# Kernel tuning notes

Hardware: AMD Instinct MI355X
Metric: run time of the kernel (lower is better)

## Reference

```python
import jax, jax.numpy as jnp
import numpy as np

N_NODES = 100000
D_IN = 128
H_DIM = 128
N_EDGES = 1600000


def _gcn_conv(x, src, dst, dinv, W, b):
    # PyG GCNConv(improved=True): h = x @ W; out = A_hat h + b,
    # A_hat = D^{-1/2} (A + 2I) D^{-1/2}
    h = x @ W                                   # [N, H]
    norm = dinv[src] * dinv[dst]                # [E]
    agg = jnp.zeros_like(h).at[dst].add(h[src] * norm[:, None])
    agg = agg + h * (2.0 * dinv * dinv)[:, None]  # self-loop, weight 2.0
    return agg + b


def setup_inputs() -> dict:
    key = jax.random.key(0)
    ks = jax.random.split(key, 12)
    s = 1.0 / np.sqrt(D_IN)
    sh = 1.0 / np.sqrt(2 * H_DIM)
    inp = {
        "x": jax.random.normal(ks[0], (N_NODES, D_IN), jnp.float32),
        "edge_index": jax.random.randint(ks[1], (2, N_EDGES), 0, N_NODES, jnp.int64),
        # GCNConv weights (in -> hidden), bias
        "Wz": jax.random.uniform(ks[2], (D_IN, H_DIM), jnp.float32, -s, s),
        "bz": jnp.zeros((H_DIM,), jnp.float32),
        "Wr": jax.random.uniform(ks[3], (D_IN, H_DIM), jnp.float32, -s, s),
        "br": jnp.zeros((H_DIM,), jnp.float32),
        "Wh": jax.random.uniform(ks[4], (D_IN, H_DIM), jnp.float32, -s, s),
        "bh": jnp.zeros((H_DIM,), jnp.float32),
        # TGCN gate linears: Linear(2h, h)
        "lzW": jax.random.uniform(ks[5], (2 * H_DIM, H_DIM), jnp.float32, -sh, sh),
        "lzb": jax.random.uniform(ks[6], (H_DIM,), jnp.float32, -sh, sh),
        "lrW": jax.random.uniform(ks[7], (2 * H_DIM, H_DIM), jnp.float32, -sh, sh),
        "lrb": jax.random.uniform(ks[8], (H_DIM,), jnp.float32, -sh, sh),
        "lhW": jax.random.uniform(ks[9], (2 * H_DIM, H_DIM), jnp.float32, -sh, sh),
        "lhb": jax.random.uniform(ks[10], (H_DIM,), jnp.float32, -sh, sh),
        # final linear2: hidden -> 1
        "W2": jax.random.uniform(ks[11], (H_DIM, 1), jnp.float32, -1 / np.sqrt(H_DIM), 1 / np.sqrt(H_DIM)),
        "b2": jnp.zeros((1,), jnp.float32),
    }
    return inp


def reference(x, edge_index, Wz, bz, Wr, br, Wh, bh, lzW, lzb, lrW, lrb, lhW, lhb, W2, b2):
    src, dst = edge_index[0], edge_index[1]
    n = x.shape[0]
    # improved GCN norm: deg includes self-loop weight 2
    deg = jnp.zeros((n,), x.dtype).at[dst].add(jnp.ones_like(src, x.dtype)) + 2.0
    dinv = jnp.where(deg > 0, deg ** -0.5, 0.0)
    # TGCN cell with H0 = 0
    H0 = jnp.zeros((n, Wz.shape[1]), x.dtype)
    Z = jax.nn.sigmoid(jnp.concatenate([_gcn_conv(x, src, dst, dinv, Wz, bz), H0], axis=1) @ lzW + lzb)
    R = jax.nn.sigmoid(jnp.concatenate([_gcn_conv(x, src, dst, dinv, Wr, br), H0], axis=1) @ lrW + lrb)
    Ht = jnp.tanh(jnp.concatenate([_gcn_conv(x, src, dst, dinv, Wh, bh), H0 * R], axis=1) @ lhW + lhb)
    H = Z * H0 + (1.0 - Z) * Ht
    # forward: relu output is discarded (y = h overwrites), then linear2
    return H @ W2 + b2
```

## Files before the change

kernel.cpp:

```cpp
#include <hip/hip_runtime.h>
#include <math.h>

#define D 128
#define BSHIFT 9
#define CAP 12288
#define EPT 13
#define P1B 481
#define XCB 12500

typedef __attribute__((ext_vector_type(8))) short s8v;
typedef __attribute__((ext_vector_type(8))) unsigned short us8;
typedef __attribute__((ext_vector_type(4))) unsigned short us4;
typedef __attribute__((ext_vector_type(4))) float f4v;

__device__ __forceinline__ float bf2f(unsigned short u) {
    union { unsigned int i; float f; } v; v.i = ((unsigned int)u) << 16; return v.f;
}
__device__ __forceinline__ unsigned short f2bf(float f) {
    union { float f; unsigned int i; } v; v.f = f;
    unsigned int r = v.i + 0x7FFFu + ((v.i >> 16) & 1u);
    return (unsigned short)(r >> 16);
}

__global__ __launch_bounds__(256) void k_combo(
    const int* __restrict__ src, const int* __restrict__ dst, int E,
    int* __restrict__ bcur, unsigned long long* __restrict__ pairs,
    const float* __restrict__ x, unsigned short* __restrict__ xb, int n4,
    const float* __restrict__ Wz, const float* __restrict__ bz,
    const float* __restrict__ lzW, const float* __restrict__ lzb,
    const float* __restrict__ Wh, const float* __restrict__ bh,
    const float* __restrict__ lhW, const float* __restrict__ lhb,
    unsigned short* __restrict__ Mt, float* __restrict__ c) {
    __shared__ int cnt[256];
    __shared__ int base[256];
    int bx = blockIdx.x, tid = threadIdx.x;

    if (bx < P1B) {
        int ed[EPT], es[EPT], rk[EPT];
        int e0 = bx * (EPT * 256) + tid;
        cnt[tid] = 0;
        __syncthreads();
        #pragma unroll
        for (int i = 0; i < EPT; ++i) {
            int e = e0 + i * 256;
            bool ok = e < E;
            ed[i] = ok ? dst[e] : 0;
            es[i] = ok ? src[e] : 0;
            rk[i] = ok ? atomicAdd(&cnt[ed[i] >> BSHIFT], 1) : 0;
        }
        __syncthreads();
        if (cnt[tid] > 0) base[tid] = tid * CAP + atomicAdd(&bcur[tid], cnt[tid]);
        __syncthreads();
        #pragma unroll
        for (int i = 0; i < EPT; ++i) {
            int e = e0 + i * 256;
            if (e < E) {
                int bk = ed[i] >> BSHIFT;
                pairs[base[bk] + rk[i]] =
                    ((unsigned long long)(unsigned int)ed[i] << 32) | (unsigned int)es[i];
            }
        }
    } else if (bx < P1B + XCB) {
        int i = (bx - P1B) * 256 + tid;
        if (i < n4) {
            float4 v = ((const float4*)x)[i];
            us4 o;
            o[0] = f2bf(v.x); o[1] = f2bf(v.y); o[2] = f2bf(v.z); o[3] = f2bf(v.w);
            ((us4*)xb)[i] = o;
        }
    } else {
        int k = bx - (P1B + XCB);
        int j = tid;
        int jj = j & 127;
        const float* W = (j < 128) ? Wz : Wh;
        const float* L = (j < 128) ? lzW : lhW;
        float s = 0.f;
        for (int t = 0; t < 128; ++t) s += W[k * 128 + t] * L[t * 128 + jj];
        Mt[(size_t)j * 128 + k] = f2bf(s);
        if (k == 0) {
            const float* b  = (j < 128) ? bz  : bh;
            const float* lb = (j < 128) ? lzb : lhb;
            float cs = lb[jj];
            for (int t = 0; t < 128; ++t) cs += b[t] * L[t * 128 + jj];
            c[j] = cs;
        }
    }
}

__global__ __launch_bounds__(256) void k_part2(const unsigned long long* __restrict__ pairs,
                                               const int* __restrict__ bcur,
                                               int NB, int N, int E,
                                               int* __restrict__ rowptr,
                                               float* __restrict__ dinv,
                                               int* __restrict__ esrc) {
    __shared__ int cnt[512];
    __shared__ int lcur[512];
    __shared__ int ts[256];
    int b = blockIdx.x, tid = threadIdx.x;
    int n0 = b << BSHIFT;
    int nn = min(N - n0, 1 << BSHIFT);
    int tot = bcur[b];
    long pbase = (long)b * CAP;

    ts[tid] = (tid < b) ? bcur[tid] : 0;
    __syncthreads();
    for (int off = 128; off > 0; off >>= 1) {
        if (tid < off) ts[tid] += ts[tid + off];
        __syncthreads();
    }
    int obase = ts[0];
    __syncthreads();

    cnt[tid] = 0; cnt[tid + 256] = 0;
    __syncthreads();
    for (int i = tid; i < tot; i += 256)
        atomicAdd(&cnt[(int)(pairs[pbase + i] >> 32) - n0], 1);
    __syncthreads();

    int a0 = cnt[2 * tid], a1 = cnt[2 * tid + 1];
    int s = a0 + a1;
    ts[tid] = s; __syncthreads();
    for (int off = 1; off < 256; off <<= 1) {
        int add = (tid >= off) ? ts[tid - off] : 0;
        __syncthreads();
        ts[tid] += add;
        __syncthreads();
    }
    int excl = ts[tid] - s;
    lcur[2 * tid]     = obase + excl;
    lcur[2 * tid + 1] = obase + excl + a0;
    if (2 * tid < nn) {
        rowptr[n0 + 2 * tid] = obase + excl;
        dinv[n0 + 2 * tid]   = rsqrtf((float)a0 + 2.0f);
    }
    if (2 * tid + 1 < nn) {
        rowptr[n0 + 2 * tid + 1] = obase + excl + a0;
        dinv[n0 + 2 * tid + 1]   = rsqrtf((float)a1 + 2.0f);
    }
    if (b == 0 && tid == 0) rowptr[N] = E;
    __syncthreads();

    for (int i = tid; i < tot; i += 256) {
        unsigned long long p = pairs[pbase + i];
        int dl = (int)(p >> 32) - n0;
        int pos = atomicAdd(&lcur[dl], 1);
        esrc[pos] = (int)(p & 0xffffffffu);
    }
}

#define ASTRIDE 136
__global__ __launch_bounds__(256, 4) void k_gather_ep(
    const unsigned short* __restrict__ xb,
    const int* __restrict__ esrc,
    const int* __restrict__ rowptr,
    const float* __restrict__ dinv,
    const unsigned short* __restrict__ Mt,
    const float* __restrict__ c, const float* __restrict__ W2,
    const float* __restrict__ b2, float* __restrict__ out, int N) {
    __shared__ unsigned short Ast[64 * ASTRIDE];
    __shared__ float pbuf[4][64];

    int tid = threadIdx.x;
    int n0 = blockIdx.x * 64;
    int hw = tid >> 5;
    int sub = tid & 31;
    int eo = sub >> 4, cs = sub & 15;

    for (int rep = 0; rep < 8; ++rep) {
        int node = n0 + rep * 8 + hw;
        int row = rep * 8 + hw;
        if (node < N) {
            int start = rowptr[node], end = rowptr[node + 1];
            float dd = dinv[node];
            float acc[8];
            #pragma unroll
            for (int j = 0; j < 8; ++j) acc[j] = 0.f;
            for (int base = start; base < end; base += 32) {
                int cntv = min(32, end - base);
                int myedge = 0; float mynorm = 0.f;
                if (sub < cntv) { myedge = esrc[base + sub]; mynorm = dinv[myedge]; }
                int pr = (cntv + 1) >> 1;
                int i = 0;
                for (; i + 3 < pr; i += 4) {
                    int i0 = 2 * i + eo;
                    int   s0 = __shfl(myedge, i0,     32); float w0 = __shfl(mynorm, i0,     32);
                    int   s1 = __shfl(myedge, i0 + 2, 32); float w1 = __shfl(mynorm, i0 + 2, 32);
                    int   s2 = __shfl(myedge, i0 + 4, 32); float w2 = __shfl(mynorm, i0 + 4, 32);
                    int   s3 = __shfl(myedge, i0 + 6, 32); float w3 = __shfl(mynorm, i0 + 6, 32);
                    us8 v0 = *(const us8*)(xb + (size_t)s0 * D + cs * 8);
                    us8 v1 = *(const us8*)(xb + (size_t)s1 * D + cs * 8);
                    us8 v2 = *(const us8*)(xb + (size_t)s2 * D + cs * 8);
                    us8 v3 = *(const us8*)(xb + (size_t)s3 * D + cs * 8);
                    #pragma unroll
                    for (int j = 0; j < 8; ++j) acc[j] += bf2f(v0[j]) * w0;
                    #pragma unroll
                    for (int j = 0; j < 8; ++j) acc[j] += bf2f(v1[j]) * w1;
                    #pragma unroll
                    for (int j = 0; j < 8; ++j) acc[j] += bf2f(v2[j]) * w2;
                    #pragma unroll
                    for (int j = 0; j < 8; ++j) acc[j] += bf2f(v3[j]) * w3;
                }
                for (; i < pr; ++i) {
                    int i0 = 2 * i + eo;
                    int   s0 = __shfl(myedge, i0, 32); float w0 = __shfl(mynorm, i0, 32);
                    us8 v0 = *(const us8*)(xb + (size_t)s0 * D + cs * 8);
                    #pragma unroll
                    for (int j = 0; j < 8; ++j) acc[j] += bf2f(v0[j]) * w0;
                }
            }
            #pragma unroll
            for (int j = 0; j < 8; ++j) acc[j] += __shfl_xor(acc[j], 16);
            if (eo == 0) {
                us8 xs = *(const us8*)(xb + (size_t)node * D + cs * 8);
                float sfac = 2.f * dd * dd;
                us8 r;
                #pragma unroll
                for (int j = 0; j < 8; ++j) r[j] = f2bf(acc[j] * dd + bf2f(xs[j]) * sfac);
                *(us8*)&Ast[row * ASTRIDE + cs * 8] = r;
            }
        } else if (eo == 0) {
            us8 z = {0, 0, 0, 0, 0, 0, 0, 0};
            *(us8*)&Ast[row * ASTRIDE + cs * 8] = z;
        }
    }
    __syncthreads();

    int wv = tid >> 6;
    int lane = tid & 63;
    int l = lane & 15, q = lane >> 4;
    int tz0 = 2 * wv;
    f4v acc[4][4];
    #pragma unroll
    for (int i = 0; i < 4; ++i)
        #pragma unroll
        for (int nt = 0; nt < 4; ++nt) acc[i][nt] = (f4v){0.f, 0.f, 0.f, 0.f};

    const unsigned short* Bb = Mt + (size_t)l * 128 + q * 8;

    #pragma unroll
    for (int ks = 0; ks < 4; ++ks) {
        s8v b[4];
        #pragma unroll
        for (int i = 0; i < 2; ++i) {
            b[i]     = *(const s8v*)(Bb + (size_t)(tz0 + i) * 16 * 128 + ks * 32);
            b[2 + i] = *(const s8v*)(Bb + (size_t)(8 + tz0 + i) * 16 * 128 + ks * 32);
        }
        #pragma unroll
        for (int nt = 0; nt < 4; ++nt) {
            s8v a = *(const s8v*)&Ast[(nt * 16 + l) * ASTRIDE + ks * 32 + q * 8];
            #pragma unroll
            for (int i = 0; i < 4; ++i)
                acc[i][nt] = __builtin_amdgcn_mfma_f32_16x16x32_bf16(a, b[i], acc[i][nt], 0, 0, 0);
        }
    }

    float p[4][4];
    #pragma unroll
    for (int nt = 0; nt < 4; ++nt)
        #pragma unroll
        for (int r = 0; r < 4; ++r) p[nt][r] = 0.f;
    #pragma unroll
    for (int i = 0; i < 2; ++i) {
        int col = (tz0 + i) * 16 + l;
        float cz = c[col], ch = c[128 + col], w2 = W2[col];
        #pragma unroll
        for (int nt = 0; nt < 4; ++nt)
            #pragma unroll
            for (int r = 0; r < 4; ++r) {
                float gz = acc[i][nt][r] + cz;
                float gh = acc[2 + i][nt][r] + ch;
                float z  = 1.f / (1.f + __expf(-gz));
                float ht = 1.f - 2.f / (__expf(2.f * gh) + 1.f);
                p[nt][r] += (1.f - z) * ht * w2;
            }
    }
    #pragma unroll
    for (int nt = 0; nt < 4; ++nt)
        #pragma unroll
        for (int r = 0; r < 4; ++r) {
            p[nt][r] += __shfl_xor(p[nt][r], 1);
            p[nt][r] += __shfl_xor(p[nt][r], 2);
            p[nt][r] += __shfl_xor(p[nt][r], 4);
            p[nt][r] += __shfl_xor(p[nt][r], 8);
        }
    if (l == 0) {
        #pragma unroll
        for (int nt = 0; nt < 4; ++nt)
            #pragma unroll
            for (int r = 0; r < 4; ++r)
                pbuf[wv][nt * 16 + q * 4 + r] = p[nt][r];
    }
    __syncthreads();
    if (tid < 64) {
        int n = n0 + tid;
        if (n < N)
            out[n] = pbuf[0][tid] + pbuf[1][tid] + pbuf[2][tid] + pbuf[3][tid] + b2[0];
    }
}

extern "C" void kernel_launch(void* const* d_in, const int* in_sizes, int n_in,
                              void* d_out, int out_size, void* d_ws, size_t ws_size,
                              hipStream_t stream) {
    const float* x    = (const float*)d_in[0];
    const int*   eidx = (const int*)d_in[1];
    const float* Wz   = (const float*)d_in[2];
    const float* bz   = (const float*)d_in[3];
    const float* Wh   = (const float*)d_in[6];
    const float* bh   = (const float*)d_in[7];
    const float* lzW  = (const float*)d_in[8];
    const float* lzb  = (const float*)d_in[9];
    const float* lhW  = (const float*)d_in[12];
    const float* lhb  = (const float*)d_in[13];
    const float* W2   = (const float*)d_in[14];
    const float* b2   = (const float*)d_in[15];
    float* out = (float*)d_out;

    int N = in_sizes[0] / D;
    int E = in_sizes[1] / 2;
    const int* src = eidx;
    const int* dst = eidx + E;
    int NB = (N + (1 << BSHIFT) - 1) >> BSHIFT;

    char* ws = (char*)d_ws;
    size_t off = 0;
    auto alloc = [&](size_t bytes) { void* p = ws + off; off += (bytes + 511) & ~(size_t)511; return p; };
    unsigned short* xb = (unsigned short*)alloc((size_t)N * D * 2);
    unsigned long long* pairs = (unsigned long long*)alloc((size_t)NB * CAP * 8);
    int*   rowptr = (int*)  alloc((size_t)(N + 1) * 4);
    float* dinv   = (float*)alloc((size_t)N * 4);
    int*   esrc   = (int*)  alloc((size_t)E * 4);
    int*   bcur   = (int*)  alloc(256 * 4);
    unsigned short* Mt = (unsigned short*)alloc(256 * 128 * 2);
    float* c      = (float*)alloc(256 * 4);

    hipMemsetAsync(bcur, 0, 256 * sizeof(int), stream);

    int n4 = N * (D / 4);
    k_combo<<<P1B + XCB + 128, 256, 0, stream>>>(
        src, dst, E, bcur, pairs, x, xb, n4,
        Wz, bz, lzW, lzb, Wh, bh, lhW, lhb, Mt, c);
    k_part2<<<NB, 256, 0, stream>>>(pairs, bcur, NB, N, E, rowptr, dinv, esrc);
    k_gather_ep<<<(N + 63) / 64, 256, 0, stream>>>(
        xb, esrc, rowptr, dinv, Mt, c, W2, b2, out, N);
}
```

Before: 249.6 us.

## Pack edge pairs into 32 bits and split gather from MFMA epilogue

Edge (dst,src) pairs are packed into a single 32-bit word, holding the local dst offset and a 17-bit src, instead of 64 bits. This halves the traffic through the bucket scratch, which now reuses the xab buffer. The fused gather+MFMA kernel is split in two. A standalone gather kernel writes the aggregated bf16 rows to a global buffer, and a separate MFMA epilogue reads them back into shared memory. The split is meant to lift the occupancy limit the fused kernel placed on the gather, at the cost of an extra 25.6MB write and read and one more launch. The 17-bit src packing only holds for N below 131072.

```diff
diff --git a/kernel.cpp b/kernel.cpp
--- a/kernel.cpp
+++ b/kernel.cpp
@@ -24,7 +24,7 @@
 
 __global__ __launch_bounds__(256) void k_combo(
     const int* __restrict__ src, const int* __restrict__ dst, int E,
-    int* __restrict__ bcur, unsigned long long* __restrict__ pairs,
+    int* __restrict__ bcur, unsigned int* __restrict__ pairs,
     const float* __restrict__ x, unsigned short* __restrict__ xb, int n4,
     const float* __restrict__ Wz, const float* __restrict__ bz,
     const float* __restrict__ lzW, const float* __restrict__ lzb,
@@ -36,7 +36,7 @@
     int bx = blockIdx.x, tid = threadIdx.x;
 
     if (bx < P1B) {
-        int ed[EPT], es[EPT], rk[EPT];
+        unsigned int pk[EPT]; int rkbk[EPT];
         int e0 = bx * (EPT * 256) + tid;
         cnt[tid] = 0;
         __syncthreads();
@@ -44,9 +44,12 @@
         for (int i = 0; i < EPT; ++i) {
             int e = e0 + i * 256;
             bool ok = e < E;
-            ed[i] = ok ? dst[e] : 0;
-            es[i] = ok ? src[e] : 0;
-            rk[i] = ok ? atomicAdd(&cnt[ed[i] >> BSHIFT], 1) : 0;
+            int d = ok ? dst[e] : 0;
+            int s = ok ? src[e] : 0;
+            int bk = d >> BSHIFT;
+            pk[i] = ((unsigned int)(d & ((1 << BSHIFT) - 1)) << 17) | (unsigned int)s;
+            int r = ok ? atomicAdd(&cnt[bk], 1) : 0;
+            rkbk[i] = (bk << 16) | r;
         }
         __syncthreads();
         if (cnt[tid] > 0) base[tid] = tid * CAP + atomicAdd(&bcur[tid], cnt[tid]);
@@ -55,9 +58,8 @@
         for (int i = 0; i < EPT; ++i) {
             int e = e0 + i * 256;
             if (e < E) {
-                int bk = ed[i] >> BSHIFT;
-                pairs[base[bk] + rk[i]] =
-                    ((unsigned long long)(unsigned int)ed[i] << 32) | (unsigned int)es[i];
+                int bk = rkbk[i] >> 16;
+                pairs[base[bk] + (rkbk[i] & 0xffff)] = pk[i];
             }
         }
     } else if (bx < P1B + XCB) {
@@ -87,7 +89,7 @@
     }
 }
 
-__global__ __launch_bounds__(256) void k_part2(const unsigned long long* __restrict__ pairs,
+__global__ __launch_bounds__(256) void k_part2(const unsigned int* __restrict__ pairs,
                                                const int* __restrict__ bcur,
                                                int NB, int N, int E,
                                                int* __restrict__ rowptr,
@@ -114,7 +116,7 @@
     cnt[tid] = 0; cnt[tid + 256] = 0;
     __syncthreads();
     for (int i = tid; i < tot; i += 256)
-        atomicAdd(&cnt[(int)(pairs[pbase + i] >> 32) - n0], 1);
+        atomicAdd(&cnt[pairs[pbase + i] >> 17], 1);
     __syncthreads();
 
     int a0 = cnt[2 * tid], a1 = cnt[2 * tid + 1];
@@ -141,20 +143,76 @@
     __syncthreads();
 
     for (int i = tid; i < tot; i += 256) {
-        unsigned long long p = pairs[pbase + i];
-        int dl = (int)(p >> 32) - n0;
+        unsigned int p = pairs[pbase + i];
+        int dl = p >> 17;
         int pos = atomicAdd(&lcur[dl], 1);
-        esrc[pos] = (int)(p & 0xffffffffu);
+        esrc[pos] = (int)(p & 0x1FFFFu);
+    }
+}
+
+__global__ __launch_bounds__(256) void k_gather(const unsigned short* __restrict__ xb,
+                                                const int* __restrict__ esrc,
+                                                const int* __restrict__ rowptr,
+                                                const float* __restrict__ dinv,
+                                                unsigned short* __restrict__ xab, int N) {
+    int node = (blockIdx.x * blockDim.x + threadIdx.x) >> 5;
+    int sub  = threadIdx.x & 31;
+    if (node >= N) return;
+    int eo = sub >> 4, cs = sub & 15;
+    int start = rowptr[node], end = rowptr[node + 1];
+    float dd = dinv[node];
+    float acc[8];
+    #pragma unroll
+    for (int j = 0; j < 8; ++j) acc[j] = 0.f;
+
+    for (int base = start; base < end; base += 32) {
+        int cnt = min(32, end - base);
+        int myedge = 0; float mynorm = 0.f;
+        if (sub < cnt) { myedge = esrc[base + sub]; mynorm = dinv[myedge]; }
+        int pairs = (cnt + 1) >> 1;
+        int i = 0;
+        for (; i + 3 < pairs; i += 4) {
+            int i0 = 2 * i + eo;
+            int   s0 = __shfl(myedge, i0,     32); float w0 = __shfl(mynorm, i0,     32);
+            int   s1 = __shfl(myedge, i0 + 2, 32); float w1 = __shfl(mynorm, i0 + 2, 32);
+            int   s2 = __shfl(myedge, i0 + 4, 32); float w2 = __shfl(mynorm, i0 + 4, 32);
+            int   s3 = __shfl(myedge, i0 + 6, 32); float w3 = __shfl(mynorm, i0 + 6, 32);
+            us8 v0 = *(const us8*)(xb + (size_t)s0 * D + cs * 8);
+            us8 v1 = *(const us8*)(xb + (size_t)s1 * D + cs * 8);
+            us8 v2 = *(const us8*)(xb + (size_t)s2 * D + cs * 8);
+            us8 v3 = *(const us8*)(xb + (size_t)s3 * D + cs * 8);
+            #pragma unroll
+            for (int j = 0; j < 8; ++j) acc[j] += bf2f(v0[j]) * w0;
+            #pragma unroll
+            for (int j = 0; j < 8; ++j) acc[j] += bf2f(v1[j]) * w1;
+            #pragma unroll
+            for (int j = 0; j < 8; ++j) acc[j] += bf2f(v2[j]) * w2;
+            #pragma unroll
+            for (int j = 0; j < 8; ++j) acc[j] += bf2f(v3[j]) * w3;
+        }
+        for (; i < pairs; ++i) {
+            int i0 = 2 * i + eo;
+            int   s0 = __shfl(myedge, i0, 32); float w0 = __shfl(mynorm, i0, 32);
+            us8 v0 = *(const us8*)(xb + (size_t)s0 * D + cs * 8);
+            #pragma unroll
+            for (int j = 0; j < 8; ++j) acc[j] += bf2f(v0[j]) * w0;
+        }
+    }
+    #pragma unroll
+    for (int j = 0; j < 8; ++j) acc[j] += __shfl_xor(acc[j], 16);
+    if (eo == 0) {
+        us8 xs = *(const us8*)(xb + (size_t)node * D + cs * 8);
+        float sfac = 2.f * dd * dd;
+        us8 r;
+        #pragma unroll
+        for (int j = 0; j < 8; ++j) r[j] = f2bf(acc[j] * dd + bf2f(xs[j]) * sfac);
+        *(us8*)(xab + (size_t)node * D + cs * 8) = r;
     }
 }
 
 #define ASTRIDE 136
-__global__ __launch_bounds__(256, 4) void k_gather_ep(
-    const unsigned short* __restrict__ xb,
-    const int* __restrict__ esrc,
-    const int* __restrict__ rowptr,
-    const float* __restrict__ dinv,
-    const unsigned short* __restrict__ Mt,
+__global__ __launch_bounds__(256, 4) void k_ep_mfma(
+    const unsigned short* __restrict__ xab, const unsigned short* __restrict__ Mt,
     const float* __restrict__ c, const float* __restrict__ W2,
     const float* __restrict__ b2, float* __restrict__ out, int N) {
     __shared__ unsigned short Ast[64 * ASTRIDE];
@@ -162,72 +220,20 @@
 
     int tid = threadIdx.x;
     int n0 = blockIdx.x * 64;
-    int hw = tid >> 5;
-    int sub = tid & 31;
-    int eo = sub >> 4, cs = sub & 15;
-
-    for (int rep = 0; rep < 8; ++rep) {
-        int node = n0 + rep * 8 + hw;
-        int row = rep * 8 + hw;
-        if (node < N) {
-            int start = rowptr[node], end = rowptr[node + 1];
-            float dd = dinv[node];
-            float acc[8];
-            #pragma unroll
-            for (int j = 0; j < 8; ++j) acc[j] = 0.f;
-            for (int base = start; base < end; base += 32) {
-                int cntv = min(32, end - base);
-                int myedge = 0; float mynorm = 0.f;
-                if (sub < cntv) { myedge = esrc[base + sub]; mynorm = dinv[myedge]; }
-                int pr = (cntv + 1) >> 1;
-                int i = 0;
-                for (; i + 3 < pr; i += 4) {
-                    int i0 = 2 * i + eo;
-                    int   s0 = __shfl(myedge, i0,     32); float w0 = __shfl(mynorm, i0,     32);
-                    int   s1 = __shfl(myedge, i0 + 2, 32); float w1 = __shfl(mynorm, i0 + 2, 32);
-                    int   s2 = __shfl(myedge, i0 + 4, 32); float w2 = __shfl(mynorm, i0 + 4, 32);
-                    int   s3 = __shfl(myedge, i0 + 6, 32); float w3 = __shfl(mynorm, i0 + 6, 32);
-                    us8 v0 = *(const us8*)(xb + (size_t)s0 * D + cs * 8);
-                    us8 v1 = *(const us8*)(xb + (size_t)s1 * D + cs * 8);
-                    us8 v2 = *(const us8*)(xb + (size_t)s2 * D + cs * 8);
-                    us8 v3 = *(const us8*)(xb + (size_t)s3 * D + cs * 8);
-                    #pragma unroll
-                    for (int j = 0; j < 8; ++j) acc[j] += bf2f(v0[j]) * w0;
-                    #pragma unroll
-                    for (int j = 0; j < 8; ++j) acc[j] += bf2f(v1[j]) * w1;
-                    #pragma unroll
-                    for (int j = 0; j < 8; ++j) acc[j] += bf2f(v2[j]) * w2;
-                    #pragma unroll
-                    for (int j = 0; j < 8; ++j) acc[j] += bf2f(v3[j]) * w3;
-                }
-                for (; i < pr; ++i) {
-                    int i0 = 2 * i + eo;
-                    int   s0 = __shfl(myedge, i0, 32); float w0 = __shfl(mynorm, i0, 32);
-                    us8 v0 = *(const us8*)(xb + (size_t)s0 * D + cs * 8);
-                    #pragma unroll
-                    for (int j = 0; j < 8; ++j) acc[j] += bf2f(v0[j]) * w0;
-                }
-            }
-            #pragma unroll
-            for (int j = 0; j < 8; ++j) acc[j] += __shfl_xor(acc[j], 16);
-            if (eo == 0) {
-                us8 xs = *(const us8*)(xb + (size_t)node * D + cs * 8);
-                float sfac = 2.f * dd * dd;
-                us8 r;
-                #pragma unroll
-                for (int j = 0; j < 8; ++j) r[j] = f2bf(acc[j] * dd + bf2f(xs[j]) * sfac);
-                *(us8*)&Ast[row * ASTRIDE + cs * 8] = r;
-            }
-        } else if (eo == 0) {
-            us8 z = {0, 0, 0, 0, 0, 0, 0, 0};
-            *(us8*)&Ast[row * ASTRIDE + cs * 8] = z;
-        }
-    }
-    __syncthreads();
-
     int wv = tid >> 6;
     int lane = tid & 63;
     int l = lane & 15, q = lane >> 4;
+
+    #pragma unroll
+    for (int j = 0; j < 4; ++j) {
+        int idx = tid + 256 * j;
+        int row = idx >> 4, c16 = idx & 15;
+        us8 v = {0, 0, 0, 0, 0, 0, 0, 0};
+        if (n0 + row < N) v = *(const us8*)(xab + (size_t)(n0 + row) * D + c16 * 8);
+        *(us8*)&Ast[row * ASTRIDE + c16 * 8] = v;
+    }
+    __syncthreads();
+
     int tz0 = 2 * wv;
     f4v acc[4][4];
     #pragma unroll
@@ -324,14 +330,15 @@
     char* ws = (char*)d_ws;
     size_t off = 0;
     auto alloc = [&](size_t bytes) { void* p = ws + off; off += (bytes + 511) & ~(size_t)511; return p; };
-    unsigned short* xb = (unsigned short*)alloc((size_t)N * D * 2);
-    unsigned long long* pairs = (unsigned long long*)alloc((size_t)NB * CAP * 8);
+    unsigned short* xb  = (unsigned short*)alloc((size_t)N * D * 2);
+    unsigned short* xab = (unsigned short*)alloc((size_t)N * D * 2);
     int*   rowptr = (int*)  alloc((size_t)(N + 1) * 4);
     float* dinv   = (float*)alloc((size_t)N * 4);
     int*   esrc   = (int*)  alloc((size_t)E * 4);
     int*   bcur   = (int*)  alloc(256 * 4);
     unsigned short* Mt = (unsigned short*)alloc(256 * 128 * 2);
     float* c      = (float*)alloc(256 * 4);
+    unsigned int* pairs = (unsigned int*)xab;
 
     hipMemsetAsync(bcur, 0, 256 * sizeof(int), stream);
 
@@ -340,6 +347,6 @@
         src, dst, E, bcur, pairs, x, xb, n4,
         Wz, bz, lzW, lzb, Wh, bh, lhW, lhb, Mt, c);
     k_part2<<<NB, 256, 0, stream>>>(pairs, bcur, NB, N, E, rowptr, dinv, esrc);
-    k_gather_ep<<<(N + 63) / 64, 256, 0, stream>>>(
-        xb, esrc, rowptr, dinv, Mt, c, W2, b2, out, N);
-}
+    k_gather<<<(N * 32 + 255) / 256, 256, 0, stream>>>(xb, esrc, rowptr, dinv, xab, N);
+    k_ep_mfma<<<(N + 63) / 64, 256, 0, stream>>>(xab, Mt, c, W2, b2, out, N);
+}
```

Measured after the change: 251.6 us. Within noise of the previous version (+0.8%).
